# Optimization experiments

Hardware: AMD Instinct MI355X
Metric: run time of the kernel (lower is better)

The kernel has to match this reference:

```python
import jax, jax.numpy as jnp
import numpy as np

B, T, D = 4, 2048, 512
H, HS = 8, 64            # n_head, head_size
E, K = 8, 2              # num_experts, top_k
CAP = int(B * T * K / E * 1.0)  # expert capacity = 2048
EPS = 1e-5


def setup_inputs() -> dict:
    key = jax.random.key(0)
    ks = jax.random.split(key, 16)
    s = lambda k, shp, fan: jax.random.normal(k, shp, jnp.float32) * (fan ** -0.5)
    return {
        "x": jax.random.normal(ks[0], (B, T, D), jnp.float32),
        "ln1_g": jnp.ones((D,), jnp.float32), "ln1_b": jnp.zeros((D,), jnp.float32),
        "Wq": s(ks[1], (H, D, HS), D), "Wk": s(ks[2], (H, D, HS), D), "Wv": s(ks[3], (H, D, HS), D),
        "Wo": s(ks[4], (D, D), D), "bo": jnp.zeros((D,), jnp.float32),
        "ln2_g": jnp.ones((D,), jnp.float32), "ln2_b": jnp.zeros((D,), jnp.float32),
        "Wg": s(ks[5], (D, E), D), "bg": jnp.zeros((E,), jnp.float32),
        "Wn": s(ks[6], (D, E), D), "bn": jnp.zeros((E,), jnp.float32),
        "W1": s(ks[7], (E, D, 4 * D), D), "b1": jnp.zeros((E, 4 * D), jnp.float32),
        "W2": s(ks[8], (E, 4 * D, D), 4 * D), "b2": jnp.zeros((E, D), jnp.float32),
    }


def _ln(x, g, b):
    m = jnp.mean(x, -1, keepdims=True)
    v = jnp.var(x, -1, keepdims=True)
    return (x - m) * jax.lax.rsqrt(v + EPS) * g + b


def _attn(h, Wq, Wk, Wv, Wo, bo):
    q = jnp.einsum('btd,hde->bhte', h, Wq)
    k = jnp.einsum('btd,hde->bhte', h, Wk)
    v = jnp.einsum('btd,hde->bhte', h, Wv)
    # NOTE: source scales by C**-0.5 with C = n_embed (not head_size)
    wei = jnp.einsum('bhte,bhse->bhts', q, k) * (D ** -0.5)
    causal = jnp.tril(jnp.ones((T, T), bool))
    wei = jnp.where(causal, wei, -jnp.inf)
    wei = jax.nn.softmax(wei, axis=-1)
    out = jnp.einsum('bhts,bhse->bhte', wei, v)              # [B,H,T,HS]
    out = out.transpose(0, 2, 1, 3).reshape(B, T, D)          # concat heads
    return out @ Wo + bo


def _moe(h, Wg, bg, Wn, bn, W1, b1, W2, b2):
    logits = h @ Wg + bg
    noise_logits = h @ Wn + bn
    noise = jax.random.normal(jax.random.key(42), logits.shape, logits.dtype) * jax.nn.softplus(noise_logits)
    noisy = logits + noise
    vals, idx = jax.lax.top_k(noisy, K)                       # [B,T,K]
    # softmax over -inf-masked sparse logits == softmax over top-k values, scattered
    gates = (jax.nn.softmax(vals, -1)[..., None] * jax.nn.one_hot(idx, E, dtype=h.dtype)).sum(-2)  # [B,T,E]
    flat_x = h.reshape(-1, D)
    flat_g = gates.reshape(-1, E)
    flat_idx = idx.reshape(-1, K)
    N = flat_x.shape[0]
    mask = (flat_idx[None] == jnp.arange(E)[:, None, None]).any(-1)   # [E,N]
    rank = jnp.cumsum(mask, axis=1) - 1
    keep = mask & (rank < CAP)                                 # first CAP tokens per expert
    slot = jnp.where(keep, rank, CAP)
    tok = jnp.arange(N, dtype=jnp.int32)

    def build(s, kp):
        buf = jnp.zeros(CAP + 1, jnp.int32).at[s].set(tok)
        vb = jnp.zeros(CAP + 1, bool).at[s].set(kp)
        return buf[:CAP], vb[:CAP]

    idx_buf, valid = jax.vmap(build)(slot, keep)               # [E,CAP]
    xg = flat_x[idx_buf]                                       # [E,CAP,D]
    mid = jax.nn.relu(jnp.einsum('ecd,edf->ecf', xg, W1) + b1[:, None, :])
    out = jnp.einsum('ecf,efd->ecd', mid, W2) + b2[:, None, :]
    gate_sel = flat_g[idx_buf, jnp.arange(E)[:, None]]         # [E,CAP]
    w = out * (gate_sel * valid.astype(h.dtype))[..., None]
    upd = jnp.zeros_like(flat_x).at[idx_buf.reshape(-1)].add(w.reshape(-1, D))
    return upd.reshape(h.shape)


def reference(x, ln1_g, ln1_b, Wq, Wk, Wv, Wo, bo, ln2_g, ln2_b,
              Wg, bg, Wn, bn, W1, b1, W2, b2):
    x = x + _attn(_ln(x, ln1_g, ln1_b), Wq, Wk, Wv, Wo, bo)
    x = x + _moe(_ln(x, ln2_g, ln2_b), Wg, bg, Wn, bn, W1, b1, W2, b2)
    return x
```

## Files before the change

### kernel.cpp

```cpp
#include <hip/hip_runtime.h>
#include <math.h>

#define TSEQ 2048
#define DD   512
#define NH   8
#define HSZ  64
#define NE   8
#define NTOK 8192
#define CAPK 2048
#define FF   2048

typedef __bf16 bf16x8 __attribute__((ext_vector_type(8)));
typedef float  f32x4  __attribute__((ext_vector_type(4)));
typedef unsigned int u32;
typedef u32 u32x4 __attribute__((ext_vector_type(4)));

__device__ __forceinline__ void gload16(const void* g, void* l){
  __builtin_amdgcn_global_load_lds((const __attribute__((address_space(1))) u32*)g,
                                   (__attribute__((address_space(3))) u32*)l, 16, 0, 0);
}

__device__ __forceinline__ u32 pkbf(float a, float b){
  unsigned short ua = __builtin_bit_cast(unsigned short, (__bf16)a);
  unsigned short ub = __builtin_bit_cast(unsigned short, (__bf16)b);
// ... 15 lines not shown
#undef TFR
  o0 = x0; o1 = x1;
}

__device__ __forceinline__ float erfinv_f(float x){
  float w = -log1pf(-x*x);
  float p;
  if (w < 5.0f){
    w -= 2.5f;
    p = 2.81022636e-08f;
    p = fmaf(p,w, 3.43273939e-07f);
    p = fmaf(p,w,-3.5233877e-06f);
    p = fmaf(p,w,-4.39150654e-06f);
    p = fmaf(p,w, 0.00021858087f);
    p = fmaf(p,w,-0.00125372503f);
    p = fmaf(p,w,-0.00417768164f);
    p = fmaf(p,w, 0.246640727f);
    p = fmaf(p,w, 1.50140941f);
  } else {
    w = sqrtf(w) - 3.0f;
    p = -0.000200214257f;
    p = fmaf(p,w, 0.000100950558f);
    p = fmaf(p,w, 0.00134934322f);
    p = fmaf(p,w,-0.00367342844f);
    p = fmaf(p,w, 0.00573950773f);
    p = fmaf(p,w,-0.0076224613f);
    p = fmaf(p,w, 0.00943887047f);
    p = fmaf(p,w, 1.00167406f);
    p = fmaf(p,w, 2.83297682f);
  }
  return p * x;
}

__global__ __launch_bounds__(256) void ln_kernel(const float* __restrict__ x,
    const float* __restrict__ gw, const float* __restrict__ bw, float* __restrict__ o)
{
  int row  = blockIdx.x*4 + threadIdx.y;
  int lane = threadIdx.x;
  const float* xr = x + (size_t)row*DD;
  float4 a = *(const float4*)(xr + lane*4);
  float4 c = *(const float4*)(xr + 256 + lane*4);
  float s  = a.x+a.y+a.z+a.w + c.x+c.y+c.z+c.w;
  float ss = a.x*a.x+a.y*a.y+a.z*a.z+a.w*a.w + c.x*c.x+c.y*c.y+c.z*c.z+c.w*c.w;
  #pragma unroll
  for (int off = 32; off; off >>= 1){ s += __shfl_xor(s, off); ss += __shfl_xor(ss, off); }
  float m   = s * (1.0f/DD);
  float var = ss * (1.0f/DD) - m*m;
  float r   = 1.0f / sqrtf(var + 1e-5f);
  float4 g1 = *(const float4*)(gw + lane*4);
  float4 b1 = *(const float4*)(bw + lane*4);
  float4 g2 = *(const float4*)(gw + 256 + lane*4);
  float4 b2 = *(const float4*)(bw + 256 + lane*4);
  float4 o1, o2;
  o1.x=(a.x-m)*r*g1.x+b1.x; o1.y=(a.y-m)*r*g1.y+b1.y; o1.z=(a.z-m)*r*g1.z+b1.z; o1.w=(a.w-m)*r*g1.w+b1.w;
  o2.x=(c.x-m)*r*g2.x+b2.x; o2.y=(c.y-m)*r*g2.y+b2.y; o2.z=(c.z-m)*r*g2.z+b2.z; o2.w=(c.w-m)*r*g2.w+b2.w;
  float* orow = o + (size_t)row*DD;
  *(float4*)(orow + lane*4)       = o1;
  *(float4*)(orow + 256 + lane*4) = o2;
}

__global__ __launch_bounds__(256) void ln_split(const float* __restrict__ x,
    const float* __restrict__ gw, const float* __restrict__ bw,
    __bf16* __restrict__ ohi, __bf16* __restrict__ olo)
{
  int row  = blockIdx.x*4 + threadIdx.y;
  int lane = threadIdx.x;
  const float* xr = x + (size_t)row*DD;
  float4 a = *(const float4*)(xr + lane*4);
  float4 c = *(const float4*)(xr + 256 + lane*4);
  float s  = a.x+a.y+a.z+a.w + c.x+c.y+c.z+c.w;
  float ss = a.x*a.x+a.y*a.y+a.z*a.z+a.w*a.w + c.x*c.x+c.y*c.y+c.z*c.z+c.w*c.w;
  #pragma unroll
  for (int off = 32; off; off >>= 1){ s += __shfl_xor(s, off); ss += __shfl_xor(ss, off); }
  float m   = s * (1.0f/DD);
  float var = ss * (1.0f/DD) - m*m;
  float r   = 1.0f / sqrtf(var + 1e-5f);
  float4 g1 = *(const float4*)(gw + lane*4);
  float4 b1 = *(const float4*)(bw + lane*4);
  float4 g2 = *(const float4*)(gw + 256 + lane*4);
  float4 b2 = *(const float4*)(bw + 256 + lane*4);
  float f1[4], f2[4];
  f1[0]=(a.x-m)*r*g1.x+b1.x; f1[1]=(a.y-m)*r*g1.y+b1.y; f1[2]=(a.z-m)*r*g1.z+b1.z; f1[3]=(a.w-m)*r*g1.w+b1.w;
  f2[0]=(c.x-m)*r*g2.x+b2.x; f2[1]=(c.y-m)*r*g2.y+b2.y; f2[2]=(c.z-m)*r*g2.z+b2.z; f2[3]=(c.w-m)*r*g2.w+b2.w;
  __bf16 h1v[4] __attribute__((aligned(8))), l1v[4] __attribute__((aligned(8)));
  __bf16 h2v[4] __attribute__((aligned(8))), l2v[4] __attribute__((aligned(8)));
  #pragma unroll
  for (int j = 0; j < 4; ++j){
    __bf16 hb = (__bf16)f1[j]; h1v[j]=hb; l1v[j]=(__bf16)(f1[j]-(float)hb);
    __bf16 hc = (__bf16)f2[j]; h2v[j]=hc; l2v[j]=(__bf16)(f2[j]-(float)hc);
  }
  size_t base = (size_t)row*DD + lane*4;
  *(uint2*)(ohi + base)       = *(const uint2*)h1v;
  *(uint2*)(olo + base)       = *(const uint2*)l1v;
// ... 25 lines not shown
    float f = t[c0+j][r];
    __bf16 h = (__bf16)f; hb[j]=h; lb[j]=(__bf16)(f-(float)h);
  }
  size_t off = (size_t)(z*64 + r)*512 + kt + c0;
  *(uint4*)(dhi+off) = ((const uint4*)hb)[0]; *(uint4*)(dhi+off+8) = ((const uint4*)hb)[1];
  *(uint4*)(dlo+off) = ((const uint4*)lb)[0]; *(uint4*)(dlo+off+8) = ((const uint4*)lb)[1];
}

__global__ __launch_bounds__(256) void transp_split(const float* __restrict__ src,
    __bf16* __restrict__ dhi, __bf16* __restrict__ dlo, int Ms, int Ns)
{
  __shared__ float t[64][65];
  int nt = blockIdx.x*64, mt = blockIdx.y*64;
  int tid = threadIdx.x;
  int r = tid>>2, c0 = (tid&3)*16;
  #pragma unroll
  for (int j = 0; j < 16; j += 4){
    float4 v = *(const float4*)&src[(size_t)(mt+r)*Ns + nt + c0 + j];
    t[r][c0+j]=v.x; t[r][c0+j+1]=v.y; t[r][c0+j+2]=v.z; t[r][c0+j+3]=v.w;
  }
  __syncthreads();
  __bf16 hb[16] __attribute__((aligned(32)));
  __bf16 lb[16] __attribute__((aligned(32)));
  #pragma unroll
  for (int j = 0; j < 16; ++j){
    float f = t[c0+j][r];
    __bf16 h = (__bf16)f; hb[j]=h; lb[j]=(__bf16)(f-(float)h);
  }
  size_t off = (size_t)(nt + r)*Ms + mt + c0;
  *(uint4*)(dhi+off) = ((const uint4*)hb)[0]; *(uint4*)(dhi+off+8) = ((const uint4*)hb)[1];
  *(uint4*)(dlo+off) = ((const uint4*)lb)[0]; *(uint4*)(dlo+off+8) = ((const uint4*)lb)[1];
}

template<int BIAS, int RES>
__global__ __launch_bounds__(256) void gemm_mfma3(
    const __bf16* __restrict__ Ahi, const __bf16* __restrict__ Alo,
    const __bf16* __restrict__ Bhi, const __bf16* __restrict__ Blo,
    const float* __restrict__ bias, const float* __restrict__ res,
    float* __restrict__ C, int M, int N, int K)
{
  __shared__ __bf16 AsH[2][4096];
  __shared__ __bf16 AsL[2][4096];
  __shared__ __bf16 BsH[2][4096];
  __shared__ __bf16 BsL[2][4096];
  int m0 = blockIdx.y*128, n0 = blockIdx.x*128;
  int tid = threadIdx.x;
  int w = tid>>6, l = tid&63;
  int wm = w>>1, wn = w&1;
  int srow = w*32 + (l>>2);
  int skb  = (l&3)<<4;
  const char* agh = (const char*)(Ahi + (size_t)(m0+srow)*K) + skb;
  const char* agl = (const char*)(Alo + (size_t)(m0+srow)*K) + skb;
  const char* bgh = (const char*)(Bhi + (size_t)(n0+srow)*K) + skb;
  const char* bgl = (const char*)(Blo + (size_t)(n0+srow)*K) + skb;
  size_t r16 = (size_t)16*K*sizeof(__bf16);

  f32x4 acc[4][4] = {};
  int rl = l & 15, kh = l >> 4;
  const __bf16* abh = &AsH[0][(wm*64 + rl)*32 + kh*8];
  const __bf16* abl = &AsL[0][(wm*64 + rl)*32 + kh*8];
  const __bf16* bbh = &BsH[0][(wn*64 + rl)*32 + kh*8];
  const __bf16* bbl = &BsL[0][(wn*64 + rl)*32 + kh*8];

  auto STAGE = [&](int bb, int kt){
    size_t o = (size_t)kt*64;
    gload16(agh+o,     &AsH[bb][w*1024]);
    gload16(agh+o+r16, &AsH[bb][w*1024+512]);
    gload16(agl+o,     &AsL[bb][w*1024]);
    gload16(agl+o+r16, &AsL[bb][w*1024+512]);
    gload16(bgh+o,     &BsH[bb][w*1024]);
    gload16(bgh+o+r16, &BsH[bb][w*1024+512]);
    gload16(bgl+o,     &BsL[bb][w*1024]);
    gload16(bgl+o+r16, &BsL[bb][w*1024+512]);
  };

  int nkt = K >> 5;
  STAGE(0, 0);
  __syncthreads();
  for (int kt = 0; kt < nkt; ++kt){
    int bb = kt & 1;
    if (kt + 1 < nkt) STAGE(bb^1, kt+1);
    bf16x8 afh[4], afl[4], bfh[4], bfl[4];
    #pragma unroll
    for (int i = 0; i < 4; ++i){
      afh[i] = *(const bf16x8*)(abh + bb*4096 + i*512);
      afl[i] = *(const bf16x8*)(abl + bb*4096 + i*512);
      bfh[i] = *(const bf16x8*)(bbh + bb*4096 + i*512);
      bfl[i] = *(const bf16x8*)(bbl + bb*4096 + i*512);
    }
    #pragma unroll
    for (int fm = 0; fm < 4; ++fm)
      #pragma unroll
      for (int fn = 0; fn < 4; ++fn){
        acc[fm][fn] = __builtin_amdgcn_mfma_f32_16x16x32_bf16(afh[fm], bfl[fn], acc[fm][fn], 0, 0, 0);
        acc[fm][fn] = __builtin_amdgcn_mfma_f32_16x16x32_bf16(afl[fm], bfh[fn], acc[fm][fn], 0, 0, 0);
        acc[fm][fn] = __builtin_amdgcn_mfma_f32_16x16x32_bf16(afh[fm], bfh[fn], acc[fm][fn], 0, 0, 0);
      }
    __syncthreads();
  }

  int ccol = l & 15, cr = (l >> 4) * 4;
  #pragma unroll
  for (int fn = 0; fn < 4; ++fn){
    int n = n0 + wn*64 + fn*16 + ccol;
    float bv = BIAS ? bias[n] : 0.0f;
    #pragma unroll
    for (int fm = 0; fm < 4; ++fm){
      int mb = m0 + wm*64 + fm*16 + cr;
      #pragma unroll
      for (int r = 0; r < 4; ++r){
        float v = acc[fm][fn][r] + bv;
        if (RES) v += res[(size_t)(mb+r)*N + n];
        C[(size_t)(mb+r)*N + n] = v;
      }
    }
  }
}

template<int STORE_BF16, int RELU>
__global__ __launch_bounds__(256) void gemm_mfma(
    const __bf16* __restrict__ A, const __bf16* __restrict__ Bt,
    const float* __restrict__ bias, void* __restrict__ Cv,
    int M, int N, int K)
{
  __shared__ __bf16 Asl[2][4096];
  __shared__ __bf16 Bsl[2][4096];
  int e = blockIdx.z;
  const __bf16* Ae = A  + (size_t)e*M*K;
  const __bf16* Be = Bt + (size_t)e*N*K;
  const float*  be = bias + (size_t)e*N;
  int m0 = blockIdx.y*128, n0 = blockIdx.x*128;
  int tid = threadIdx.x;
  int w = tid>>6, l = tid&63;
  int wm = w>>1, wn = w&1;
  int srow = w*32 + (l>>2);
  int skb  = (l&3)<<4;
  const char* ag = (const char*)(Ae + (size_t)(m0 + srow)*K) + skb;
  const char* bg = (const char*)(Be + (size_t)(n0 + srow)*K) + skb;
  size_t r16 = (size_t)16*K*sizeof(__bf16);

  f32x4 acc[4][4] = {};
  int rl = l & 15, kh = l >> 4;
  const __bf16* abase = &Asl[0][(wm*64 + rl)*32 + kh*8];
  const __bf16* bbase = &Bsl[0][(wn*64 + rl)*32 + kh*8];

  auto STAGE = [&](int bb, int kt){
    size_t o = (size_t)kt*64;
    gload16(ag+o,     &Asl[bb][w*1024]);
    gload16(ag+o+r16, &Asl[bb][w*1024+512]);
    gload16(bg+o,     &Bsl[bb][w*1024]);
    gload16(bg+o+r16, &Bsl[bb][w*1024+512]);
  };

  int nkt = K >> 5;
  STAGE(0, 0);
  __syncthreads();
  for (int kt = 0; kt < nkt; ++kt){
    int bb = kt & 1;
    if (kt + 1 < nkt) STAGE(bb^1, kt+1);
    bf16x8 af[4], bf[4];
    #pragma unroll
    for (int i = 0; i < 4; ++i){
      af[i] = *(const bf16x8*)(abase + bb*4096 + i*512);
      bf[i] = *(const bf16x8*)(bbase + bb*4096 + i*512);
    }
    #pragma unroll
    for (int fm = 0; fm < 4; ++fm)
      #pragma unroll
      for (int fn = 0; fn < 4; ++fn)
        acc[fm][fn] = __builtin_amdgcn_mfma_f32_16x16x32_bf16(af[fm], bf[fn], acc[fm][fn], 0, 0, 0);
    __syncthreads();
  }

  int ccol = l & 15, cr = (l >> 4) * 4;
  char* Ce = (char*)Cv + (size_t)e*M*N*(STORE_BF16 ? 2 : 4);
  #pragma unroll
  for (int fn = 0; fn < 4; ++fn){
    int n = n0 + wn*64 + fn*16 + ccol;
    float bv = be[n];
    #pragma unroll
    for (int fm = 0; fm < 4; ++fm){
      int mb = m0 + wm*64 + fm*16 + cr;
      #pragma unroll
      for (int r = 0; r < 4; ++r){
        float v = acc[fm][fn][r] + bv;
        if (RELU) v = fmaxf(v, 0.f);
        if (STORE_BF16) ((__bf16*)Ce)[(size_t)(mb+r)*N + n] = (__bf16)v;
        else            ((float*)Ce)[(size_t)(mb+r)*N + n] = v;
      }
    }
  }
}

__global__ __launch_bounds__(256) void transp_conv(const float* __restrict__ src,
    __bf16* __restrict__ dst, int Ms, int Ns)
{
  __shared__ __bf16 t[64][72];
  int e = blockIdx.z;
  const float* s = src + (size_t)e*Ms*Ns;
  __bf16* d = dst + (size_t)e*Ms*Ns;
  int mt = blockIdx.y*64, nt = blockIdx.x*64;
  int tid = threadIdx.x;
  int r = tid>>2, c0 = (tid&3)*16;
  #pragma unroll
  for (int j = 0; j < 16; j += 4){
    float4 v = *(const float4*)&s[(size_t)(mt+r)*Ns + nt + c0 + j];
    t[r][c0+j]   = (__bf16)v.x; t[r][c0+j+1] = (__bf16)v.y;
    t[r][c0+j+2] = (__bf16)v.z; t[r][c0+j+3] = (__bf16)v.w;
  }
  __syncthreads();
  __bf16 tmp[16] __attribute__((aligned(32)));
  #pragma unroll
  for (int j = 0; j < 16; ++j) tmp[j] = t[c0+j][r];
  uint4* dp = (uint4*)&d[(size_t)(nt+r)*Ms + mt + c0];
  dp[0] = ((const uint4*)tmp)[0];
  dp[1] = ((const uint4*)tmp)[1];
}

__global__ __launch_bounds__(256) void convert_kv(const float* __restrict__ qkv,
    __bf16* __restrict__ khi, __bf16* __restrict__ klo,
    __bf16* __restrict__ vthi, __bf16* __restrict__ vtlo)
{
  int t0 = blockIdx.x*64;
  int bh = blockIdx.y;
  int b = bh >> 3, h = bh & 7;
  int tid = threadIdx.x;
  {
    int r = tid >> 2, e0 = (tid & 3) * 16;
    const float* src = qkv + ((size_t)(b*TSEQ + t0 + r))*1536 + 512 + h*64 + e0;
    __bf16 hi[16] __attribute__((aligned(16)));
    __bf16 lo[16] __attribute__((aligned(16)));
    #pragma unroll
    for (int j = 0; j < 16; j += 4){
      float4 v = *(const float4*)(src + j);
      float f[4] = {v.x, v.y, v.z, v.w};
      #pragma unroll
      for (int q = 0; q < 4; ++q){
        __bf16 hb = (__bf16)f[q];
        hi[j+q] = hb; lo[j+q] = (__bf16)(f[q] - (float)hb);
      }
    }
    size_t off = ((size_t)(bh*TSEQ + t0 + r))*64 + e0;
    *(uint4*)(khi + off)     = ((const uint4*)hi)[0];
    *(uint4*)(khi + off + 8) = ((const uint4*)hi)[1];
    *(uint4*)(klo + off)     = ((const uint4*)lo)[0];
    *(uint4*)(klo + off + 8) = ((const uint4*)lo)[1];
  }
  {
    int key0 = (tid & 15) * 4, e0 = (tid >> 4) * 4;
    float4 v[4];
    #pragma unroll
    for (int j = 0; j < 4; ++j)
      v[j] = *(const float4*)(qkv + ((size_t)(b*TSEQ + t0 + key0 + j))*1536 + 1024 + h*64 + e0);
    float col[4][4];
    col[0][0]=v[0].x; col[0][1]=v[1].x; col[0][2]=v[2].x; col[0][3]=v[3].x;
    col[1][0]=v[0].y; col[1][1]=v[1].y; col[1][2]=v[2].y; col[1][3]=v[3].y;
    col[2][0]=v[0].z; col[2][1]=v[1].z; col[2][2]=v[2].z; col[2][3]=v[3].z;
    col[3][0]=v[0].w; col[3][1]=v[1].w; col[3][2]=v[2].w; col[3][3]=v[3].w;
    #pragma unroll
    for (int kk = 0; kk < 4; ++kk){
      __bf16 hi[4] __attribute__((aligned(8)));
      __bf16 lo[4] __attribute__((aligned(8)));
      #pragma unroll
      for (int j = 0; j < 4; ++j){
        __bf16 hb = (__bf16)col[kk][j];
        hi[j] = hb; lo[j] = (__bf16)(col[kk][j] - (float)hb);
      }
      size_t off = ((size_t)(bh*64 + e0 + kk))*TSEQ + t0 + key0;
      *(uint2*)(vthi + off) = *(const uint2*)hi;
      *(uint2*)(vtlo + off) = *(const uint2*)lo;
    }
  }
}

__global__ __launch_bounds__(512) void attn_mfma(const float* __restrict__ qkv,
    const __bf16* __restrict__ khi_g, const __bf16* __restrict__ klo_g,
    const __bf16* __restrict__ vthi_g, const __bf16* __restrict__ vtlo_g,
    __bf16* __restrict__ ahi, __bf16* __restrict__ alo)
{
  __shared__ __align__(16) char ldsbuf[65536];
  int bh = blockIdx.x;
  int qtA = blockIdx.y, qtB = 15 - qtA;
  int b = bh >> 3, h = bh & 7;
  int tid = threadIdx.x;
  int w = tid >> 6, l = tid & 63;
  int g = l >> 4, r = l & 15;
  int sA = r + 32*(g & 1);
  int sB = sA + 16;
  int ghalf = g >> 1;
  const float qsc = 0.04419417382415922f * 1.4426950408889634f;

  int qb[2]; qb[0] = qtA*128 + w*16; qb[1] = qtB*128 + (7-w)*16;
  int kdiag[2]; kdiag[0] = qb[0] >> 6; kdiag[1] = qb[1] >> 6;

  bf16x8 qhi[2][2], qlo[2][2];
  #pragma unroll
  for (int qf = 0; qf < 2; ++qf)
    #pragma unroll
    for (int ks = 0; ks < 2; ++ks){
      const float* src = qkv + ((size_t)(b*TSEQ + qb[qf] + r))*1536 + h*64 + ks*32 + g*8;
      float4 v0 = *(const float4*)src;
      float4 v1 = *(const float4*)(src + 4);
      float f[8] = {v0.x,v0.y,v0.z,v0.w,v1.x,v1.y,v1.z,v1.w};
      bf16x8 hi, lo;
      #pragma unroll
      for (int i = 0; i < 8; ++i){
        float fs = f[i] * qsc;
        __bf16 hb = (__bf16)fs;
        hi[i] = hb; lo[i] = (__bf16)(fs - (float)hb);
      }
      qhi[qf][ks] = hi; qlo[qf][ks] = lo;
    }

  f32x4 ot[4][2] = {};
  float m_r[2] = {-INFINITY, -INFINITY};
  float l_r[2] = {0.f, 0.f};

  int nkt = 2*qtB + 2;
  size_t kbase = (size_t)bh*TSEQ*64;
  size_t vbase = (size_t)bh*64*TSEQ;

  auto STAGE = [&](int buf, int kt){
    int row = tid >> 3, cc = tid & 7;
    int sw = (cc ^ (row & 7)) * 8;
    char* d = ldsbuf + buf*32768 + (w << 10);
    gload16(khi_g  + kbase + (size_t)(kt*64 + row)*64 + sw, d);
    gload16(klo_g  + kbase + (size_t)(kt*64 + row)*64 + sw, d + 8192);
    gload16(vthi_g + vbase + (size_t)row*TSEQ + kt*64 + sw,  d + 16384);
    gload16(vtlo_g + vbase + (size_t)row*TSEQ + kt*64 + sw,  d + 24576);
  };

  STAGE(0, 0);
  __syncthreads();

  for (int kt = 0; kt < nkt; ++kt){
    int buf = kt & 1;
    if (kt + 1 < nkt) STAGE(buf ^ 1, kt + 1);

    bool act[2];
    act[0] = (kt <= kdiag[0]);
    act[1] = (kt <= kdiag[1]);

    const char* K0 = ldsbuf + buf*32768;
    const char* K1 = K0 + 8192;
    const char* V0 = K0 + 16384;
    const char* V1 = K0 + 24576;

    f32x4 s[4][2] = {};
    #pragma unroll
    for (int kf = 0; kf < 4; ++kf){
      int rowk = kf*16 + r;
      int rsw = (rowk & 7) << 4;
      #pragma unroll
      for (int ks = 0; ks < 2; ++ks){
        int off = rowk*128 + ((((ks*4 + g) << 4)) ^ rsw);
        bf16x8 khf = *(const bf16x8*)(K0 + off);
        bf16x8 klf = *(const bf16x8*)(K1 + off);
        #pragma unroll
        for (int qf = 0; qf < 2; ++qf){
          if (act[qf]){
            s[kf][qf] = __builtin_amdgcn_mfma_f32_16x16x32_bf16(khf, qlo[qf][ks], s[kf][qf], 0,0,0);
            s[kf][qf] = __builtin_amdgcn_mfma_f32_16x16x32_bf16(klf, qhi[qf][ks], s[kf][qf], 0,0,0);
            s[kf][qf] = __builtin_amdgcn_mfma_f32_16x16x32_bf16(khf, qhi[qf][ks], s[kf][qf], 0,0,0);
          }
        }
      }
    }

    u32 phi[4][2][2], plo[4][2][2];
    #pragma unroll
    for (int qf = 0; qf < 2; ++qf){
      if (act[qf]){
        int q = qb[qf] + r;
        float p[4][4];
        float mx = -INFINITY;
        if (kt == kdiag[qf]){
          #pragma unroll
          for (int kf = 0; kf < 4; ++kf)
            #pragma unroll
            for (int e = 0; e < 4; ++e){
              int key = kt*64 + kf*16 + g*4 + e;
              float sv = (key <= q) ? s[kf][qf][e] : -INFINITY;
              p[kf][e] = sv;
              mx = fmaxf(mx, sv);
            }
        } else {
          #pragma unroll
          for (int kf = 0; kf < 4; ++kf)
            #pragma unroll
            for (int e = 0; e < 4; ++e){
              float sv = s[kf][qf][e];
              p[kf][e] = sv;
              mx = fmaxf(mx, sv);
            }
        }
        mx = fmaxf(mx, __shfl_xor(mx, 16));
        mx = fmaxf(mx, __shfl_xor(mx, 32));
        if (__any(mx > m_r[qf])){
          float mn = fmaxf(m_r[qf], mx);
          float fj = exp2f(m_r[qf] - mn);
          m_r[qf] = mn;
          l_r[qf] *= fj;
          #pragma unroll
          for (int ef = 0; ef < 4; ++ef)
            #pragma unroll
            for (int e = 0; e < 4; ++e)
              ot[ef][qf][e] *= fj;
        }
        float ts = 0.f;
        #pragma unroll
        for (int kf = 0; kf < 4; ++kf)
          #pragma unroll
          for (int e = 0; e < 4; ++e){
            float pv = exp2f(p[kf][e] - m_r[qf]);
            p[kf][e] = pv; ts += pv;
          }
        ts += __shfl_xor(ts, 16); ts += __shfl_xor(ts, 32);
        l_r[qf] += ts;
        #pragma unroll
        for (int kf = 0; kf < 4; ++kf){
          __bf16 h0=(__bf16)p[kf][0], h1=(__bf16)p[kf][1], h2=(__bf16)p[kf][2], h3=(__bf16)p[kf][3];
          phi[kf][qf][0] = pkbf(p[kf][0], p[kf][1]);
          phi[kf][qf][1] = pkbf(p[kf][2], p[kf][3]);
          plo[kf][qf][0] = pkbf(p[kf][0]-(float)h0, p[kf][1]-(float)h1);
          plo[kf][qf][1] = pkbf(p[kf][2]-(float)h2, p[kf][3]-(float)h3);
        }
      }
    }

    #pragma unroll
    for (int ks = 0; ks < 2; ++ks){
      u32x4 pbh[2], pbl[2];
      #pragma unroll
      for (int qf = 0; qf < 2; ++qf){
        if (act[qf]){
          #pragma unroll
          for (int p2 = 0; p2 < 2; ++p2){
            u32 hA0 = (u32)__shfl((int)phi[2*ks  ][qf][p2], sA);
            u32 hA1 = (u32)__shfl((int)phi[2*ks+1][qf][p2], sA);
            u32 hB0 = (u32)__shfl((int)phi[2*ks  ][qf][p2], sB);
            u32 hB1 = (u32)__shfl((int)phi[2*ks+1][qf][p2], sB);
            pbh[qf][p2]   = ghalf ? hA1 : hA0;
            pbh[qf][2+p2] = ghalf ? hB1 : hB0;
            u32 lA0 = (u32)__shfl((int)plo[2*ks  ][qf][p2], sA);
            u32 lA1 = (u32)__shfl((int)plo[2*ks+1][qf][p2], sA);
            u32 lB0 = (u32)__shfl((int)plo[2*ks  ][qf][p2], sB);
            u32 lB1 = (u32)__shfl((int)plo[2*ks+1][qf][p2], sB);
            pbl[qf][p2]   = ghalf ? lA1 : lA0;
            pbl[qf][2+p2] = ghalf ? lB1 : lB0;
          }
        }
      }
      #pragma unroll
      for (int ef = 0; ef < 4; ++ef){
        int rowv = ef*16 + r;
        int off = rowv*128 + ((((ks*4 + g) << 4)) ^ ((rowv & 7) << 4));
        bf16x8 vhf = *(const bf16x8*)(V0 + off);
        bf16x8 vlf = *(const bf16x8*)(V1 + off);
        #pragma unroll
        for (int qf = 0; qf < 2; ++qf){
          if (act[qf]){
            bf16x8 ph = __builtin_bit_cast(bf16x8, pbh[qf]);
            bf16x8 pl = __builtin_bit_cast(bf16x8, pbl[qf]);
            ot[ef][qf] = __builtin_amdgcn_mfma_f32_16x16x32_bf16(vhf, pl, ot[ef][qf], 0,0,0);
            ot[ef][qf] = __builtin_amdgcn_mfma_f32_16x16x32_bf16(vlf, ph, ot[ef][qf], 0,0,0);
            ot[ef][qf] = __builtin_amdgcn_mfma_f32_16x16x32_bf16(vhf, ph, ot[ef][qf], 0,0,0);
          }
        }
      }
    }
    __syncthreads();
  }

  float* Osh = (float*)ldsbuf;
  #pragma unroll
  for (int qf = 0; qf < 2; ++qf){
    float inv = 1.0f / l_r[qf];
    int qloc = (qf ? (7-w) : w)*16 + r;
    #pragma unroll
    for (int ef = 0; ef < 4; ++ef)
      #pragma unroll
      for (int e = 0; e < 4; ++e)
        Osh[qloc*68 + ef*16 + g*4 + e] = ot[ef][qf][e] * inv;
    __syncthreads();
    {
      int qt = qf ? qtB : qtA;
      int q = tid >> 2, e0 = (tid & 3)*16;
      const float* srow = Osh + q*68 + e0;
      size_t base = ((size_t)(b*TSEQ + qt*128 + q))*DD + h*64 + e0;
      #pragma unroll
      for (int j = 0; j < 4; ++j){
        float4 v = *(const float4*)(srow + j*4);
        float f[4] = {v.x, v.y, v.z, v.w};
        __bf16 hb[4] __attribute__((aligned(8)));
        __bf16 lb[4] __attribute__((aligned(8)));
        #pragma unroll
        for (int q2 = 0; q2 < 4; ++q2){
          __bf16 h2b = (__bf16)f[q2];
          hb[q2] = h2b; lb[q2] = (__bf16)(f[q2] - (float)h2b);
        }
        *(uint2*)(ahi + base + j*4) = *(const uint2*)hb;
        *(uint2*)(alo + base + j*4) = *(const uint2*)lb;
      }
    }
    __syncthreads();
  }
}

__global__ __launch_bounds__(256) void router_kernel(const float* __restrict__ h2,
    const float* __restrict__ Wg, const float* __restrict__ bg,
    const float* __restrict__ Wn, const float* __restrict__ bn,
    int* __restrict__ idx0, int* __restrict__ idx1,
    float* __restrict__ g0, float* __restrict__ g1)
{
  int wid = threadIdx.x >> 6, lane = threadIdx.x & 63;
  int tok = blockIdx.x*4 + wid;
  const float* xr = h2 + (size_t)tok*DD;
  float ag[8] = {0,0,0,0,0,0,0,0}, an[8] = {0,0,0,0,0,0,0,0};
  for (int d = lane; d < DD; d += 64){
    float xv = xr[d];
    const float* wg = Wg + d*8;
    const float* wn = Wn + d*8;
    #pragma unroll
    for (int e = 0; e < 8; ++e){ ag[e] = fmaf(xv, wg[e], ag[e]); an[e] = fmaf(xv, wn[e], an[e]); }
  }
  #pragma unroll
  for (int off = 32; off; off >>= 1){
    #pragma unroll
    for (int e = 0; e < 8; ++e){ ag[e] += __shfl_xor(ag[e], off); an[e] += __shfl_xor(an[e], off); }
  }
  __shared__ float ns[4][8];
  if (lane < 8){
    int e = lane;
    float lg = ag[e] + bg[e];
    float nl = an[e] + bn[e];
    float sp = fmaxf(nl, 0.f) + log1pf(expf(-fabsf(nl)));
    unsigned i = (unsigned)(tok*8 + e);
    unsigned r0b, r1b;
    threefry2x32(0u, i, r0b, r1b);
    unsigned bits = r0b ^ r1b;
    float f = __uint_as_float((bits >> 9) | 0x3f800000u) - 1.0f;
    float u = fmaf(f, 2.0f, -0.99999994f);
    u = fmaxf(u, -0.99999994f);
    float z = 1.41421356f * erfinv_f(u);
    ns[wid][e] = lg + z*sp;
  }
  __syncthreads();
  if (lane == 0){
    float v0 = -INFINITY; int i0 = 0;
    #pragma unroll
    for (int e = 0; e < 8; ++e){ float v = ns[wid][e]; if (v > v0){ v0 = v; i0 = e; } }
    float v1 = -INFINITY; int i1 = 0;
    #pragma unroll
    for (int e = 0; e < 8; ++e){ if (e != i0){ float v = ns[wid][e]; if (v > v1){ v1 = v; i1 = e; } } }
    float dexp = expf(v1 - v0);
    float ssum = 1.0f + dexp;
    idx0[tok] = i0; idx1[tok] = i1;
    g0[tok] = 1.0f/ssum; g1[tok] = dexp/ssum;
  }
}

__global__ __launch_bounds__(256) void route_scan(const int* __restrict__ idx0,
    const int* __restrict__ idx1, int* __restrict__ idx_buf, int* __restrict__ tok_slot)
{
  int e = blockIdx.x, tid = threadIdx.x;
  for (int i = tid; i < CAPK; i += 256) idx_buf[e*CAPK + i] = 0;
  __syncthreads();
  int base = tid * 32;
  int cnt = 0;
  for (int j = 0; j < 32; ++j){ int t = base + j; cnt += (idx0[t]==e || idx1[t]==e) ? 1 : 0; }
  __shared__ int ps[256];
  ps[tid] = cnt; __syncthreads();
  for (int off = 1; off < 256; off <<= 1){
    int add = (tid >= off) ? ps[tid - off] : 0;
    __syncthreads();
    ps[tid] += add;
    __syncthreads();
  }
  int slot = ps[tid] - cnt;
  for (int j = 0; j < 32; ++j){
    int t = base + j;
    int k = (idx0[t]==e) ? 0 : ((idx1[t]==e) ? 1 : -1);
    if (k >= 0){
      if (slot < CAPK){ idx_buf[e*CAPK + slot] = t; tok_slot[t*2 + k] = slot; }
      else            { tok_slot[t*2 + k] = -1; }
      slot++;
    }
  }
}

__global__ __launch_bounds__(128) void gather_bf16(const float* __restrict__ h2,
    const int* __restrict__ idx_buf, __bf16* __restrict__ xg)
{
  int ec = blockIdx.x;
  int tok = idx_buf[ec];
  float4 v = ((const float4*)(h2 + (size_t)tok*DD))[threadIdx.x];
  __bf16 o[4] __attribute__((aligned(8)));
  o[0]=(__bf16)v.x; o[1]=(__bf16)v.y; o[2]=(__bf16)v.z; o[3]=(__bf16)v.w;
  ((uint2*)(xg + (size_t)ec*DD))[threadIdx.x] = *(const uint2*)o;
}

__global__ __launch_bounds__(128) void combine_kernel(const float* __restrict__ x1,
    const __bf16* __restrict__ eout, const int* __restrict__ idx0, const int* __restrict__ idx1,
    const float* __restrict__ g0, const float* __restrict__ g1,
    const int* __restrict__ tok_slot, float* __restrict__ outp)
{
  int n = blockIdx.x, t = threadIdx.x;
  float4 acc = *(const float4*)(x1 + (size_t)n*DD + t*4);
  #pragma unroll
  for (int k = 0; k < 2; ++k){
    int s = tok_slot[n*2 + k];
    if (s >= 0){
      int e  = (k==0) ? idx0[n] : idx1[n];
      float g = (k==0) ? g0[n] : g1[n];
      __bf16 vb[4] __attribute__((aligned(8)));
      *(uint2*)vb = *(const uint2*)(eout + ((size_t)(e*CAPK + s))*DD + t*4);
      acc.x = fmaf(g, (float)vb[0], acc.x); acc.y = fmaf(g, (float)vb[1], acc.y);
      acc.z = fmaf(g, (float)vb[2], acc.z); acc.w = fmaf(g, (float)vb[3], acc.w);
    }
  }
  *(float4*)(outp + (size_t)n*DD + t*4) = acc;
}

extern "C" void kernel_launch(void* const* d_in, const int* in_sizes, int n_in,
                              void* d_out, int out_size, void* d_ws, size_t ws_size,
                              hipStream_t stream)
{
  const float* x    = (const float*)d_in[0];
  const float* ln1g = (const float*)d_in[1];
  const float* ln1b = (const float*)d_in[2];
  const float* Wq   = (const float*)d_in[3];
  const float* Wk   = (const float*)d_in[4];
  const float* Wv   = (const float*)d_in[5];
  const float* Wo   = (const float*)d_in[6];
  const float* bo   = (const float*)d_in[7];
  const float* ln2g = (const float*)d_in[8];
  const float* ln2b = (const float*)d_in[9];
  const float* Wg   = (const float*)d_in[10];
  const float* bg   = (const float*)d_in[11];
  const float* Wn   = (const float*)d_in[12];
  const float* bn   = (const float*)d_in[13];
  const float* W1   = (const float*)d_in[14];
  const float* b1   = (const float*)d_in[15];
  const float* W2   = (const float*)d_in[16];
  const float* b2   = (const float*)d_in[17];
  float* out = (float*)d_out;
  char* ws = (char*)d_ws;
  const size_t MB = 1u << 20;

  __bf16* h1hi   = (__bf16*)(ws);
  __bf16* h1lo   = (__bf16*)(ws + 8*MB);
  __bf16* attnhi = (__bf16*)(ws);
  __bf16* attnlo = (__bf16*)(ws + 8*MB);
  float*  h2     = (float*)(ws);
  float*  qkv    = (float*)(ws + 16*MB);
  __bf16* W1T    = (__bf16*)(ws + 16*MB);
  __bf16* W2T    = (__bf16*)(ws + 32*MB);
  __bf16* xg     = (__bf16*)(ws + 48*MB);
  float*  x1     = (float*)(ws + 64*MB);
  __bf16* Khi    = (__bf16*)(ws + 80*MB);
  __bf16* Klo    = (__bf16*)(ws + 88*MB);
  __bf16* Vthi   = (__bf16*)(ws + 96*MB);
  __bf16* Vtlo   = (__bf16*)(ws + 104*MB);
  __bf16* Bqh    = (__bf16*)(ws + 80*MB);
  __bf16* Bql    = (__bf16*)(ws + 82*MB);
  __bf16* eoutb  = (__bf16*)(ws + 80*MB);
  __bf16* mid    = (__bf16*)(ws + 112*MB);
  __bf16* WoTh   = (__bf16*)(ws + 144*MB);
  __bf16* WoTl   = (__bf16*)(ws + 144*MB + 512*1024);
  char*   smallp = ws + 145*MB;
  int*   idx0     = (int*)smallp;
  int*   idx1     = idx0 + NTOK;
  float* g0       = (float*)(idx1 + NTOK);
  float* g1       = g0 + NTOK;
  int*   tok_slot = (int*)(g1 + NTOK);
  int*   idx_buf  = tok_slot + NTOK*2;

  ln_split<<<dim3(NTOK/4), dim3(64,4), 0, stream>>>(x, ln1g, ln1b, h1hi, h1lo);
  pack_qkv_split<<<dim3(8,24), 256, 0, stream>>>(Wq, Wk, Wv, Bqh, Bql);
  transp_split<<<dim3(8,8), 256, 0, stream>>>(Wo, WoTh, WoTl, DD, DD);
  gemm_mfma3<0,0><<<dim3(12,64), 256, 0, stream>>>(h1hi, h1lo, Bqh, Bql, nullptr, nullptr, qkv, NTOK, 1536, DD);
  convert_kv<<<dim3(TSEQ/64, 32), 256, 0, stream>>>(qkv, Khi, Klo, Vthi, Vtlo);
  attn_mfma<<<dim3(32, 8), 512, 0, stream>>>(qkv, Khi, Klo, Vthi, Vtlo, attnhi, attnlo);
  gemm_mfma3<1,1><<<dim3(4,64), 256, 0, stream>>>(attnhi, attnlo, WoTh, WoTl, bo, x, x1, NTOK, DD, DD);
  ln_kernel<<<dim3(NTOK/4), dim3(64,4), 0, stream>>>(x1, ln2g, ln2b, h2);
  transp_conv<<<dim3(32,8,NE), 256, 0, stream>>>(W1, W1T, DD, FF);
  transp_conv<<<dim3(8,32,NE), 256, 0, stream>>>(W2, W2T, FF, DD);
  router_kernel<<<dim3(NTOK/4), 256, 0, stream>>>(h2, Wg, bg, Wn, bn, idx0, idx1, g0, g1);
  route_scan<<<dim3(NE), 256, 0, stream>>>(idx0, idx1, idx_buf, tok_slot);
  gather_bf16<<<dim3(NE*CAPK), 128, 0, stream>>>(h2, idx_buf, xg);
  for (int gg = 0; gg < 2; ++gg){
    gemm_mfma<1,1><<<dim3(FF/128, CAPK/128, 4), 256, 0, stream>>>(
        xg + (size_t)gg*4*CAPK*DD, W1T + (size_t)gg*4*DD*FF, b1 + (size_t)gg*4*FF,
        mid, CAPK, FF, DD);
    gemm_mfma<1,0><<<dim3(DD/128, CAPK/128, 4), 256, 0, stream>>>(
        mid, W2T + (size_t)gg*4*FF*DD, b2 + (size_t)gg*4*DD,
        eoutb + (size_t)gg*4*CAPK*DD, CAPK, DD, FF);
  }
  combine_kernel<<<dim3(NTOK), 128, 0, stream>>>(x1, eoutb, idx0, idx1, g0, g1, tok_slot, out);
}
```

Baseline: 436.5 us.

## Fuse QKV split/convert into GEMM epilogue, fuse LN2 with router, add setprio

The QKV GEMM now writes scaled Q, K and transposed V directly as bf16 hi/lo pairs in its epilogue, which removes the fp32 qkv buffer, the convert_kv kernel and the Q conversion inside attention. LN2 is fused into the router kernel, which also emits bf16 activations so the gather becomes a plain copy. s_setprio hints are placed around the MFMA loops, and the online-softmax rescale now fires only when the max grows by more than 8, which skips rescale work but lets exponentials grow larger. The epilogue stores for Q and K are scalar and strided, and the workspace layout is reshuffled to fit the new buffers.

```diff
diff --git a/kernel.cpp b/kernel.cpp
--- a/kernel.cpp
+++ b/kernel.cpp
@@ -71,33 +71,6 @@
   return p * x;
 }
 
-__global__ __launch_bounds__(256) void ln_kernel(const float* __restrict__ x,
-    const float* __restrict__ gw, const float* __restrict__ bw, float* __restrict__ o)
-{
-  int row  = blockIdx.x*4 + threadIdx.y;
-  int lane = threadIdx.x;
-  const float* xr = x + (size_t)row*DD;
-  float4 a = *(const float4*)(xr + lane*4);
-  float4 c = *(const float4*)(xr + 256 + lane*4);
-  float s  = a.x+a.y+a.z+a.w + c.x+c.y+c.z+c.w;
-  float ss = a.x*a.x+a.y*a.y+a.z*a.z+a.w*a.w + c.x*c.x+c.y*c.y+c.z*c.z+c.w*c.w;
-  #pragma unroll
-  for (int off = 32; off; off >>= 1){ s += __shfl_xor(s, off); ss += __shfl_xor(ss, off); }
-  float m   = s * (1.0f/DD);
-  float var = ss * (1.0f/DD) - m*m;
-  float r   = 1.0f / sqrtf(var + 1e-5f);
-  float4 g1 = *(const float4*)(gw + lane*4);
-  float4 b1 = *(const float4*)(bw + lane*4);
-  float4 g2 = *(const float4*)(gw + 256 + lane*4);
-  float4 b2 = *(const float4*)(bw + 256 + lane*4);
-  float4 o1, o2;
-  o1.x=(a.x-m)*r*g1.x+b1.x; o1.y=(a.y-m)*r*g1.y+b1.y; o1.z=(a.z-m)*r*g1.z+b1.z; o1.w=(a.w-m)*r*g1.w+b1.w;
-  o2.x=(c.x-m)*r*g2.x+b2.x; o2.y=(c.y-m)*r*g2.y+b2.y; o2.z=(c.z-m)*r*g2.z+b2.z; o2.w=(c.w-m)*r*g2.w+b2.w;
-  float* orow = o + (size_t)row*DD;
-  *(float4*)(orow + lane*4)       = o1;
-  *(float4*)(orow + 256 + lane*4) = o2;
-}
-
 __global__ __launch_bounds__(256) void ln_split(const float* __restrict__ x,
     const float* __restrict__ gw, const float* __restrict__ bw,
     __bf16* __restrict__ ohi, __bf16* __restrict__ olo)
@@ -189,12 +162,15 @@
   *(uint4*)(dlo+off) = ((const uint4*)lb)[0]; *(uint4*)(dlo+off+8) = ((const uint4*)lb)[1];
 }
 
-template<int BIAS, int RES>
+template<int MODE>
 __global__ __launch_bounds__(256) void gemm_mfma3(
     const __bf16* __restrict__ Ahi, const __bf16* __restrict__ Alo,
     const __bf16* __restrict__ Bhi, const __bf16* __restrict__ Blo,
-    const float* __restrict__ bias, const float* __restrict__ res,
-    float* __restrict__ C, int M, int N, int K)
+    const float* __restrict__ bias, const float* __restrict__ res, float* __restrict__ C,
+    __bf16* __restrict__ qh, __bf16* __restrict__ ql,
+    __bf16* __restrict__ kh, __bf16* __restrict__ kl,
+    __bf16* __restrict__ vth, __bf16* __restrict__ vtl,
+    int M, int N, int K)
 {
   __shared__ __bf16 AsH[2][4096];
   __shared__ __bf16 AsL[2][4096];
@@ -213,11 +189,11 @@
   size_t r16 = (size_t)16*K*sizeof(__bf16);
 
   f32x4 acc[4][4] = {};
-  int rl = l & 15, kh = l >> 4;
-  const __bf16* abh = &AsH[0][(wm*64 + rl)*32 + kh*8];
-  const __bf16* abl = &AsL[0][(wm*64 + rl)*32 + kh*8];
-  const __bf16* bbh = &BsH[0][(wn*64 + rl)*32 + kh*8];
-  const __bf16* bbl = &BsL[0][(wn*64 + rl)*32 + kh*8];
+  int rl = l & 15, kh_ = l >> 4;
+  const __bf16* abh = &AsH[0][(wm*64 + rl)*32 + kh_*8];
+  const __bf16* abl = &AsL[0][(wm*64 + rl)*32 + kh_*8];
+  const __bf16* bbh = &BsH[0][(wn*64 + rl)*32 + kh_*8];
+  const __bf16* bbl = &BsL[0][(wn*64 + rl)*32 + kh_*8];
 
   auto STAGE = [&](int bb, int kt){
     size_t o = (size_t)kt*64;
@@ -245,6 +221,7 @@
       bfh[i] = *(const bf16x8*)(bbh + bb*4096 + i*512);
       bfl[i] = *(const bf16x8*)(bbl + bb*4096 + i*512);
     }
+    __builtin_amdgcn_s_setprio(1);
     #pragma unroll
     for (int fm = 0; fm < 4; ++fm)
       #pragma unroll
@@ -253,22 +230,61 @@
         acc[fm][fn] = __builtin_amdgcn_mfma_f32_16x16x32_bf16(afl[fm], bfh[fn], acc[fm][fn], 0, 0, 0);
         acc[fm][fn] = __builtin_amdgcn_mfma_f32_16x16x32_bf16(afh[fm], bfh[fn], acc[fm][fn], 0, 0, 0);
       }
+    __builtin_amdgcn_s_setprio(0);
     __syncthreads();
   }
 
   int ccol = l & 15, cr = (l >> 4) * 4;
-  #pragma unroll
-  for (int fn = 0; fn < 4; ++fn){
-    int n = n0 + wn*64 + fn*16 + ccol;
-    float bv = BIAS ? bias[n] : 0.0f;
-    #pragma unroll
-    for (int fm = 0; fm < 4; ++fm){
-      int mb = m0 + wm*64 + fm*16 + cr;
-      #pragma unroll
-      for (int r = 0; r < 4; ++r){
-        float v = acc[fm][fn][r] + bv;
-        if (RES) v += res[(size_t)(mb+r)*N + n];
-        C[(size_t)(mb+r)*N + n] = v;
+  if (MODE == 0){
+    #pragma unroll
+    for (int fn = 0; fn < 4; ++fn){
+      int n = n0 + wn*64 + fn*16 + ccol;
+      float bv = bias[n];
+      #pragma unroll
+      for (int fm = 0; fm < 4; ++fm){
+        int mb = m0 + wm*64 + fm*16 + cr;
+        #pragma unroll
+        for (int r = 0; r < 4; ++r){
+          float v = acc[fm][fn][r] + bv + res[(size_t)(mb+r)*N + n];
+          C[(size_t)(mb+r)*N + n] = v;
+        }
+      }
+    }
+  } else {
+    int b = m0 >> 11;
+    int tb = (m0 & 2047) + wm*64 + cr;
+    int sel = n0 >> 9;
+    const float qsc = 0.04419417382415922f * 1.4426950408889634f;
+    #pragma unroll
+    for (int fn = 0; fn < 4; ++fn){
+      int n = n0 + wn*64 + fn*16 + ccol;
+      int hh = (n >> 6) & 7, e = n & 63;
+      size_t bh = (size_t)(b*8 + hh);
+      #pragma unroll
+      for (int fm = 0; fm < 4; ++fm){
+        int t0 = tb + fm*16;
+        if (sel == 2){
+          __bf16 hv[4] __attribute__((aligned(8))), lv[4] __attribute__((aligned(8)));
+          #pragma unroll
+          for (int r = 0; r < 4; ++r){
+            float v = acc[fm][fn][r];
+            __bf16 hb = (__bf16)v; hv[r] = hb; lv[r] = (__bf16)(v - (float)hb);
+          }
+          size_t off = (bh*64 + e)*TSEQ + t0;
+          *(uint2*)(vth + off) = *(const uint2*)hv;
+          *(uint2*)(vtl + off) = *(const uint2*)lv;
+        } else {
+          __bf16* dh = sel ? kh : qh;
+          __bf16* dl = sel ? kl : ql;
+          float sc = sel ? 1.0f : qsc;
+          #pragma unroll
+          for (int r = 0; r < 4; ++r){
+            float v = acc[fm][fn][r] * sc;
+            __bf16 hb = (__bf16)v;
+            size_t off = (bh*TSEQ + t0 + r)*64 + e;
+            dh[off] = hb; dl[off] = (__bf16)(v - (float)hb);
+          }
+        }
       }
     }
   }
@@ -321,11 +337,13 @@
       af[i] = *(const bf16x8*)(abase + bb*4096 + i*512);
       bf[i] = *(const bf16x8*)(bbase + bb*4096 + i*512);
     }
+    __builtin_amdgcn_s_setprio(1);
     #pragma unroll
     for (int fm = 0; fm < 4; ++fm)
       #pragma unroll
       for (int fn = 0; fn < 4; ++fn)
         acc[fm][fn] = __builtin_amdgcn_mfma_f32_16x16x32_bf16(af[fm], bf[fn], acc[fm][fn], 0, 0, 0);
+    __builtin_amdgcn_s_setprio(0);
     __syncthreads();
   }
 
@@ -374,63 +392,8 @@
   dp[1] = ((const uint4*)tmp)[1];
 }
 
-__global__ __launch_bounds__(256) void convert_kv(const float* __restrict__ qkv,
-    __bf16* __restrict__ khi, __bf16* __restrict__ klo,
-    __bf16* __restrict__ vthi, __bf16* __restrict__ vtlo)
-{
-  int t0 = blockIdx.x*64;
-  int bh = blockIdx.y;
-  int b = bh >> 3, h = bh & 7;
-  int tid = threadIdx.x;
-  {
-    int r = tid >> 2, e0 = (tid & 3) * 16;
-    const float* src = qkv + ((size_t)(b*TSEQ + t0 + r))*1536 + 512 + h*64 + e0;
-    __bf16 hi[16] __attribute__((aligned(16)));
-    __bf16 lo[16] __attribute__((aligned(16)));
-    #pragma unroll
-    for (int j = 0; j < 16; j += 4){
-      float4 v = *(const float4*)(src + j);
-      float f[4] = {v.x, v.y, v.z, v.w};
-      #pragma unroll
-      for (int q = 0; q < 4; ++q){
-        __bf16 hb = (__bf16)f[q];
-        hi[j+q] = hb; lo[j+q] = (__bf16)(f[q] - (float)hb);
-      }
-    }
-    size_t off = ((size_t)(bh*TSEQ + t0 + r))*64 + e0;
-    *(uint4*)(khi + off)     = ((const uint4*)hi)[0];
-    *(uint4*)(khi + off + 8) = ((const uint4*)hi)[1];
-    *(uint4*)(klo + off)     = ((const uint4*)lo)[0];
-    *(uint4*)(klo + off + 8) = ((const uint4*)lo)[1];
-  }
-  {
-    int key0 = (tid & 15) * 4, e0 = (tid >> 4) * 4;
-    float4 v[4];
-    #pragma unroll
-    for (int j = 0; j < 4; ++j)
-      v[j] = *(const float4*)(qkv + ((size_t)(b*TSEQ + t0 + key0 + j))*1536 + 1024 + h*64 + e0);
-    float col[4][4];
-    col[0][0]=v[0].x; col[0][1]=v[1].x; col[0][2]=v[2].x; col[0][3]=v[3].x;
-    col[1][0]=v[0].y; col[1][1]=v[1].y; col[1][2]=v[2].y; col[1][3]=v[3].y;
-    col[2][0]=v[0].z; col[2][1]=v[1].z; col[2][2]=v[2].z; col[2][3]=v[3].z;
-    col[3][0]=v[0].w; col[3][1]=v[1].w; col[3][2]=v[2].w; col[3][3]=v[3].w;
-    #pragma unroll
-    for (int kk = 0; kk < 4; ++kk){
-      __bf16 hi[4] __attribute__((aligned(8)));
-      __bf16 lo[4] __attribute__((aligned(8)));
-      #pragma unroll
-      for (int j = 0; j < 4; ++j){
-        __bf16 hb = (__bf16)col[kk][j];
-        hi[j] = hb; lo[j] = (__bf16)(col[kk][j] - (float)hb);
-      }
-      size_t off = ((size_t)(bh*64 + e0 + kk))*TSEQ + t0 + key0;
-      *(uint2*)(vthi + off) = *(const uint2*)hi;
-      *(uint2*)(vtlo + off) = *(const uint2*)lo;
-    }
-  }
-}
-
-__global__ __launch_bounds__(512) void attn_mfma(const float* __restrict__ qkv,
+__global__ __launch_bounds__(512) void attn_mfma(
+    const __bf16* __restrict__ qhi_g, const __bf16* __restrict__ qlo_g,
     const __bf16* __restrict__ khi_g, const __bf16* __restrict__ klo_g,
     const __bf16* __restrict__ vthi_g, const __bf16* __restrict__ vtlo_g,
     __bf16* __restrict__ ahi, __bf16* __restrict__ alo)
@@ -438,14 +401,13 @@
   __shared__ __align__(16) char ldsbuf[65536];
   int bh = blockIdx.x;
   int qtA = blockIdx.y, qtB = 15 - qtA;
-  int b = bh >> 3, h = bh & 7;
+  int b = bh >> 3;
   int tid = threadIdx.x;
   int w = tid >> 6, l = tid & 63;
   int g = l >> 4, r = l & 15;
   int sA = r + 32*(g & 1);
   int sB = sA + 16;
   int ghalf = g >> 1;
-  const float qsc = 0.04419417382415922f * 1.4426950408889634f;
 
   int qb[2]; qb[0] = qtA*128 + w*16; qb[1] = qtB*128 + (7-w)*16;
   int kdiag[2]; kdiag[0] = qb[0] >> 6; kdiag[1] = qb[1] >> 6;
@@ -455,18 +417,9 @@
   for (int qf = 0; qf < 2; ++qf)
     #pragma unroll
     for (int ks = 0; ks < 2; ++ks){
-      const float* src = qkv + ((size_t)(b*TSEQ + qb[qf] + r))*1536 + h*64 + ks*32 + g*8;
-      float4 v0 = *(const float4*)src;
-      float4 v1 = *(const float4*)(src + 4);
-      float f[8] = {v0.x,v0.y,v0.z,v0.w,v1.x,v1.y,v1.z,v1.w};
-      bf16x8 hi, lo;
-      #pragma unroll
-      for (int i = 0; i < 8; ++i){
-        float fs = f[i] * qsc;
-        __bf16 hb = (__bf16)fs;
-        hi[i] = hb; lo[i] = (__bf16)(fs - (float)hb);
-      }
-      qhi[qf][ks] = hi; qlo[qf][ks] = lo;
+      size_t qoff = ((size_t)bh*TSEQ + qb[qf] + r)*64 + ks*32 + g*8;
+      qhi[qf][ks] = *(const bf16x8*)(qhi_g + qoff);
+      qlo[qf][ks] = *(const bf16x8*)(qlo_g + qoff);
     }
 
   f32x4 ot[4][2] = {};
@@ -504,6 +457,7 @@
     const char* V1 = K0 + 24576;
 
     f32x4 s[4][2] = {};
+    __builtin_amdgcn_s_setprio(1);
     #pragma unroll
     for (int kf = 0; kf < 4; ++kf){
       int rowk = kf*16 + r;
@@ -523,6 +477,7 @@
         }
       }
     }
+    __builtin_amdgcn_s_setprio(0);
 
     u32 phi[4][2][2], plo[4][2][2];
     #pragma unroll
@@ -553,7 +508,7 @@
         }
         mx = fmaxf(mx, __shfl_xor(mx, 16));
         mx = fmaxf(mx, __shfl_xor(mx, 32));
-        if (__any(mx > m_r[qf])){
+        if (__any(mx > m_r[qf] + 8.0f)){
           float mn = fmaxf(m_r[qf], mx);
           float fj = exp2f(m_r[qf] - mn);
           m_r[qf] = mn;
@@ -608,6 +563,7 @@
           }
         }
       }
+      __builtin_amdgcn_s_setprio(1);
       #pragma unroll
       for (int ef = 0; ef < 4; ++ef){
         int rowv = ef*16 + r;
@@ -625,6 +581,7 @@
           }
         }
       }
+      __builtin_amdgcn_s_setprio(0);
     }
     __syncthreads();
   }
@@ -644,6 +601,7 @@
       int qt = qf ? qtB : qtA;
       int q = tid >> 2, e0 = (tid & 3)*16;
       const float* srow = Osh + q*68 + e0;
+      int h = bh & 7;
       size_t base = ((size_t)(b*TSEQ + qt*128 + q))*DD + h*64 + e0;
       #pragma unroll
       for (int j = 0; j < 4; ++j){
@@ -664,22 +622,55 @@
   }
 }
 
-__global__ __launch_bounds__(256) void router_kernel(const float* __restrict__ h2,
+__global__ __launch_bounds__(256) void routerln_kernel(const float* __restrict__ x1,
+    const float* __restrict__ gw, const float* __restrict__ bw,
     const float* __restrict__ Wg, const float* __restrict__ bg,
     const float* __restrict__ Wn, const float* __restrict__ bn,
+    __bf16* __restrict__ h2b,
     int* __restrict__ idx0, int* __restrict__ idx1,
     float* __restrict__ g0, float* __restrict__ g1)
 {
   int wid = threadIdx.x >> 6, lane = threadIdx.x & 63;
   int tok = blockIdx.x*4 + wid;
-  const float* xr = h2 + (size_t)tok*DD;
+  const float* xr = x1 + (size_t)tok*DD;
+  float4 a = *(const float4*)(xr + lane*4);
+  float4 c = *(const float4*)(xr + 256 + lane*4);
+  float s  = a.x+a.y+a.z+a.w + c.x+c.y+c.z+c.w;
+  float ss = a.x*a.x+a.y*a.y+a.z*a.z+a.w*a.w + c.x*c.x+c.y*c.y+c.z*c.z+c.w*c.w;
+  #pragma unroll
+  for (int off = 32; off; off >>= 1){ s += __shfl_xor(s, off); ss += __shfl_xor(ss, off); }
+  float m   = s * (1.0f/DD);
+  float var = ss * (1.0f/DD) - m*m;
+  float rr  = 1.0f / sqrtf(var + 1e-5f);
+  float4 g1v = *(const float4*)(gw + lane*4);
+  float4 b1v = *(const float4*)(bw + lane*4);
+  float4 g2v = *(const float4*)(gw + 256 + lane*4);
+  float4 b2v = *(const float4*)(bw + 256 + lane*4);
+  float f1[4], f2[4];
+  f1[0]=(a.x-m)*rr*g1v.x+b1v.x; f1[1]=(a.y-m)*rr*g1v.y+b1v.y; f1[2]=(a.z-m)*rr*g1v.z+b1v.z; f1[3]=(a.w-m)*rr*g1v.w+b1v.w;
+  f2[0]=(c.x-m)*rr*g2v.x+b2v.x; f2[1]=(c.y-m)*rr*g2v.y+b2v.y; f2[2]=(c.z-m)*rr*g2v.z+b2v.z; f2[3]=(c.w-m)*rr*g2v.w+b2v.w;
+  {
+    __bf16 h1v[4] __attribute__((aligned(8)));
+    __bf16 h2v[4] __attribute__((aligned(8)));
+    #pragma unroll
+    for (int j = 0; j < 4; ++j){ h1v[j] = (__bf16)f1[j]; h2v[j] = (__bf16)f2[j]; }
+    size_t base = (size_t)tok*DD + lane*4;
+    *(uint2*)(h2b + base)       = *(const uint2*)h1v;
+    *(uint2*)(h2b + base + 256) = *(const uint2*)h2v;
+  }
   float ag[8] = {0,0,0,0,0,0,0,0}, an[8] = {0,0,0,0,0,0,0,0};
-  for (int d = lane; d < DD; d += 64){
-    float xv = xr[d];
-    const float* wg = Wg + d*8;
-    const float* wn = Wn + d*8;
-    #pragma unroll
-    for (int e = 0; e < 8; ++e){ ag[e] = fmaf(xv, wg[e], ag[e]); an[e] = fmaf(xv, wn[e], an[e]); }
+  int d1 = lane*4, d2 = 256 + lane*4;
+  #pragma unroll
+  for (int j = 0; j < 4; ++j){
+    const float* wg1 = Wg + (size_t)(d1+j)*8;
+    const float* wn1 = Wn + (size_t)(d1+j)*8;
+    const float* wg2 = Wg + (size_t)(d2+j)*8;
+    const float* wn2 = Wn + (size_t)(d2+j)*8;
+    #pragma unroll
+    for (int e = 0; e < 8; ++e){
+      ag[e] = fmaf(f1[j], wg1[e], ag[e]); an[e] = fmaf(f1[j], wn1[e], an[e]);
+      ag[e] = fmaf(f2[j], wg2[e], ag[e]); an[e] = fmaf(f2[j], wn2[e], an[e]);
+    }
   }
   #pragma unroll
   for (int off = 32; off; off >>= 1){
@@ -746,15 +737,13 @@
   }
 }
 
-__global__ __launch_bounds__(128) void gather_bf16(const float* __restrict__ h2,
+__global__ __launch_bounds__(128) void gather_b(const __bf16* __restrict__ h2b,
     const int* __restrict__ idx_buf, __bf16* __restrict__ xg)
 {
   int ec = blockIdx.x;
   int tok = idx_buf[ec];
-  float4 v = ((const float4*)(h2 + (size_t)tok*DD))[threadIdx.x];
-  __bf16 o[4] __attribute__((aligned(8)));
-  o[0]=(__bf16)v.x; o[1]=(__bf16)v.y; o[2]=(__bf16)v.z; o[3]=(__bf16)v.w;
-  ((uint2*)(xg + (size_t)ec*DD))[threadIdx.x] = *(const uint2*)o;
+  ((uint2*)(xg + (size_t)ec*DD))[threadIdx.x] =
+      ((const uint2*)(h2b + (size_t)tok*DD))[threadIdx.x];
 }
 
 __global__ __launch_bounds__(128) void combine_kernel(const float* __restrict__ x1,
@@ -809,22 +798,23 @@
   __bf16* h1lo   = (__bf16*)(ws + 8*MB);
   __bf16* attnhi = (__bf16*)(ws);
   __bf16* attnlo = (__bf16*)(ws + 8*MB);
-  float*  h2     = (float*)(ws);
-  float*  qkv    = (float*)(ws + 16*MB);
+  __bf16* h2b    = (__bf16*)(ws);
+  __bf16* Qhi    = (__bf16*)(ws + 16*MB);
+  __bf16* Qlo    = (__bf16*)(ws + 24*MB);
+  __bf16* Khi    = (__bf16*)(ws + 32*MB);
+  __bf16* Klo    = (__bf16*)(ws + 40*MB);
+  __bf16* Vthi   = (__bf16*)(ws + 48*MB);
+  __bf16* Vtlo   = (__bf16*)(ws + 56*MB);
   __bf16* W1T    = (__bf16*)(ws + 16*MB);
   __bf16* W2T    = (__bf16*)(ws + 32*MB);
   __bf16* xg     = (__bf16*)(ws + 48*MB);
   float*  x1     = (float*)(ws + 64*MB);
-  __bf16* Khi    = (__bf16*)(ws + 80*MB);
-  __bf16* Klo    = (__bf16*)(ws + 88*MB);
-  __bf16* Vthi   = (__bf16*)(ws + 96*MB);
-  __bf16* Vtlo   = (__bf16*)(ws + 104*MB);
-  __bf16* Bqh    = (__bf16*)(ws + 80*MB);
-  __bf16* Bql    = (__bf16*)(ws + 82*MB);
   __bf16* eoutb  = (__bf16*)(ws + 80*MB);
+  __bf16* Bqh    = (__bf16*)(ws + 96*MB);
+  __bf16* Bql    = (__bf16*)(ws + 98*MB);
+  __bf16* WoTh   = (__bf16*)(ws + 100*MB);
+  __bf16* WoTl   = (__bf16*)(ws + 101*MB);
   __bf16* mid    = (__bf16*)(ws + 112*MB);
-  __bf16* WoTh   = (__bf16*)(ws + 144*MB);
-  __bf16* WoTl   = (__bf16*)(ws + 144*MB + 512*1024);
   char*   smallp = ws + 145*MB;
   int*   idx0     = (int*)smallp;
   int*   idx1     = idx0 + NTOK;
@@ -836,16 +826,17 @@
   ln_split<<<dim3(NTOK/4), dim3(64,4), 0, stream>>>(x, ln1g, ln1b, h1hi, h1lo);
   pack_qkv_split<<<dim3(8,24), 256, 0, stream>>>(Wq, Wk, Wv, Bqh, Bql);
   transp_split<<<dim3(8,8), 256, 0, stream>>>(Wo, WoTh, WoTl, DD, DD);
-  gemm_mfma3<0,0><<<dim3(12,64), 256, 0, stream>>>(h1hi, h1lo, Bqh, Bql, nullptr, nullptr, qkv, NTOK, 1536, DD);
-  convert_kv<<<dim3(TSEQ/64, 32), 256, 0, stream>>>(qkv, Khi, Klo, Vthi, Vtlo);
-  attn_mfma<<<dim3(32, 8), 512, 0, stream>>>(qkv, Khi, Klo, Vthi, Vtlo, attnhi, attnlo);
-  gemm_mfma3<1,1><<<dim3(4,64), 256, 0, stream>>>(attnhi, attnlo, WoTh, WoTl, bo, x, x1, NTOK, DD, DD);
-  ln_kernel<<<dim3(NTOK/4), dim3(64,4), 0, stream>>>(x1, ln2g, ln2b, h2);
+  gemm_mfma3<1><<<dim3(12,64), 256, 0, stream>>>(h1hi, h1lo, Bqh, Bql,
+      nullptr, nullptr, nullptr, Qhi, Qlo, Khi, Klo, Vthi, Vtlo, NTOK, 1536, DD);
+  attn_mfma<<<dim3(32, 8), 512, 0, stream>>>(Qhi, Qlo, Khi, Klo, Vthi, Vtlo, attnhi, attnlo);
+  gemm_mfma3<0><<<dim3(4,64), 256, 0, stream>>>(attnhi, attnlo, WoTh, WoTl,
+      bo, x, x1, nullptr, nullptr, nullptr, nullptr, nullptr, nullptr, NTOK, DD, DD);
+  routerln_kernel<<<dim3(NTOK/4), 256, 0, stream>>>(x1, ln2g, ln2b, Wg, bg, Wn, bn,
+      h2b, idx0, idx1, g0, g1);
   transp_conv<<<dim3(32,8,NE), 256, 0, stream>>>(W1, W1T, DD, FF);
   transp_conv<<<dim3(8,32,NE), 256, 0, stream>>>(W2, W2T, FF, DD);
-  router_kernel<<<dim3(NTOK/4), 256, 0, stream>>>(h2, Wg, bg, Wn, bn, idx0, idx1, g0, g1);
   route_scan<<<dim3(NE), 256, 0, stream>>>(idx0, idx1, idx_buf, tok_slot);
-  gather_bf16<<<dim3(NE*CAPK), 128, 0, stream>>>(h2, idx_buf, xg);
+  gather_b<<<dim3(NE*CAPK), 128, 0, stream>>>(h2b, idx_buf, xg);
   for (int gg = 0; gg < 2; ++gg){
     gemm_mfma<1,1><<<dim3(FF/128, CAPK/128, 4), 256, 0, stream>>>(
         xg + (size_t)gg*4*CAPK*DD, W1T + (size_t)gg*4*DD*FF, b1 + (size_t)gg*4*FF,
```

Result: slower. 452.0 us (+3.5%).
